# Performance work log

Hardware: AMD Instinct MI355X
Metric: run time of the kernel (lower is better)

## Reference

```python
import jax, jax.numpy as jnp
import numpy as np

N_NODES = 50000


def _add_self_loops(edge_index, num_nodes):
    loop = jnp.arange(num_nodes, dtype=edge_index.dtype)
    row = jnp.concatenate([edge_index[0], loop])
    col = jnp.concatenate([edge_index[1], loop])
    return row, col


def _gcn_norm(row, col, num_nodes):
    # deg computed on target index with unit edge weights (PyG gcn_norm)
    deg = jax.ops.segment_sum(jnp.ones_like(col, dtype=jnp.float32), col,
                              num_segments=num_nodes)
    dis = jnp.where(deg > 0, jax.lax.rsqrt(jnp.maximum(deg, 1.0)), 0.0)
    return dis[row] * dis[col]  # [E]


def _gcn_conv(x, W, b, row, col, norm, num_nodes):
    h = x @ W                                  # dense transform first (PyG order)
    msg = h[row] * norm[:, None]               # gather + normalize
    out = jax.ops.segment_sum(msg, col, num_segments=num_nodes)  # scatter-add
    return out + b


def setup_inputs() -> dict:
    key = jax.random.key(0)
    ks = jax.random.split(key, 10)
    E = 800000
    x = jax.random.normal(ks[0], (N_NODES, 29), dtype=jnp.float32)
    edge_index = jax.random.randint(ks[1], (2, E), 0, N_NODES, dtype=jnp.int64)

    def glorot(k, fan_in, fan_out):
        s = jnp.sqrt(2.0 / (fan_in + fan_out)).astype(jnp.float32)
        return jax.random.normal(k, (fan_in, fan_out), dtype=jnp.float32) * s

    return {
        "x": x, "edge_index": edge_index,
        "W1": glorot(ks[2], 29, 96),  "b1": jnp.zeros((96,), jnp.float32),
        "W2": glorot(ks[3], 96, 128), "b2": jnp.zeros((128,), jnp.float32),
        "W3": glorot(ks[4], 128, 64), "b3": jnp.zeros((64,), jnp.float32),
        "W4": glorot(ks[5], 64, 32),  "b4": jnp.zeros((32,), jnp.float32),
    }


def reference(x, edge_index, W1, b1, W2, b2, W3, b3, W4, b4):
    row, col = _add_self_loops(edge_index, N_NODES)
    norm = _gcn_norm(row, col, N_NODES)  # same graph -> same norm for all layers
    h = _gcn_conv(x, W1, b1, row, col, norm, N_NODES)
    h = jax.nn.relu(h)
    # dropout(p=0.4) is identity in eval mode
    h = _gcn_conv(h, W2, b2, row, col, norm, N_NODES)
    h = _gcn_conv(h, W3, b3, row, col, norm, N_NODES)
    h = _gcn_conv(h, W4, b4, row, col, norm, N_NODES)
    return h
```

## Files before the change

### kernel.cpp

```cpp
#include <hip/hip_runtime.h>


constexpr int NN  = 50000;
constexpr int CAP = 64;
constexpr int AGB = (NN * 8 + 255) / 256;
constexpr int C1B = (NN + 255) / 256;
constexpr int PREPB = (NN * 32 + 64 + 255) / 256;
constexpr int W34XB = 17;
constexpr int W234XB = 13;
constexpr int PGB = 128;
constexpr int SLICE = (800000 + PGB - 1) / PGB;

typedef unsigned short u16;

__global__ void place_x_kernel(const int* __restrict__ row, const int* __restrict__ col,
                               int* __restrict__ cnt, u16* __restrict__ ell, int E) {
    const int g  = blockIdx.x & 7;
    const int bi = blockIdx.x >> 3;
    const int e0 = bi * SLICE;
    int e1 = e0 + SLICE; if (e1 > E) e1 = E;
    for (int e = e0 + threadIdx.x; e < e1; e += 256) {
        const int c = col[e];
        if ((unsigned)c >= (unsigned)NN || ((c >> 6) & 7) != g) continue;
        const int r = row[e];
        if ((unsigned)r >= (unsigned)NN) continue;
        const int pos = atomicAdd(&cnt[c], 1);
        if (pos < CAP) ell[c * CAP + pos] = (u16)r;
    }
}

__global__ void prep_all_kernel(const int* __restrict__ cnt, u16* __restrict__ ell,
                                const float* __restrict__ x, float* __restrict__ dis,
                                float* __restrict__ Ba, float* __restrict__ Bb,
                                float* __restrict__ c1d,
                                const float* __restrict__ W3, const float* __restrict__ W4,
                                const float* __restrict__ b3,
                                float* __restrict__ W34, float* __restrict__ v1) {
    if (blockIdx.x >= PREPB) {
        const int wid = (blockIdx.x - PREPB) * 256 + threadIdx.x;
        if (wid < 4096) {
            const int r = wid >> 5, j = wid & 31;
            float a = 0.f;
#pragma unroll 8
            for (int k = 0; k < 64; ++k) a = fmaf(W3[r * 64 + k], W4[k * 32 + j], a);
            W34[wid] = a;
        } else if (wid < 4128) {
            const int j = wid - 4096;
            float a = 0.f;
#pragma unroll 8
            for (int k = 0; k < 64; ++k) a = fmaf(b3[k], W4[k * 32 + j], a);
            v1[j] = a;
        }
        return;
    }
    const int idx = blockIdx.x * blockDim.x + threadIdx.x;
    if (idx < NN * 32) {
        const int n = idx >> 5, f = idx & 31;
        int m = cnt[n]; if (m > CAP) m = CAP;
        const float d = rsqrtf((float)m + 1.0f);
        Ba[idx] = (f < 29) ? x[n * 29 + f] * d : 0.f;
        if (f == 31) dis[n] = d;
        if (f == 30) {
            int mp = (m + 7) & ~7; if (mp > CAP) mp = CAP;
            for (int k = m; k < mp; ++k) ell[n * CAP + k] = (u16)NN;
        }
    } else {
        const int i = idx - NN * 32;
        if (i < 32) { Ba[NN * 32 + i] = 0.f; Bb[NN * 32 + i] = 0.f; }
        else if (i == 32) dis[NN] = 0.f;
        else if (i == 33) c1d[NN] = 0.f;
    }
}

template<int MODE>
__device__ __forceinline__ void agg32_body(const float* __restrict__ hs,
                                           const int* __restrict__ cnt,
                                           const u16* __restrict__ ell,
                                           const float* __restrict__ dis,
                                           const float* __restrict__ c1,
                                           const float* __restrict__ c2,
                                           const float* __restrict__ v1,
                                           const float* __restrict__ v2,
                                           const float* __restrict__ bv,
                                           float* __restrict__ out) {
    const int idx = blockIdx.x * blockDim.x + threadIdx.x;
    if (idx >= NN * 8) return;
    const int n = idx >> 3, c = idx & 7;
    const float4* hpc = (const float4*)hs + c;
    float4 acc = hpc[n * 8];
    int m = cnt[n]; if (m > CAP) m = CAP;
    const int m8 = (m + 7) >> 3;
    const int4* ip = (const int4*)(ell + n * CAP);
    for (int t = 0; t < m8; ++t) {
        const int4 s = ip[t];
        const unsigned ux = (unsigned)s.x, uy = (unsigned)s.y;
        const unsigned uz = (unsigned)s.z, uw = (unsigned)s.w;
        const float4 g0 = hpc[(ux & 0xFFFFu) * 8], g1 = hpc[(ux >> 16) * 8];
        const float4 g2 = hpc[(uy & 0xFFFFu) * 8], g3 = hpc[(uy >> 16) * 8];
        const float4 g4 = hpc[(uz & 0xFFFFu) * 8], g5 = hpc[(uz >> 16) * 8];
        const float4 g6 = hpc[(uw & 0xFFFFu) * 8], g7 = hpc[(uw >> 16) * 8];
        acc.x += ((g0.x + g1.x) + (g2.x + g3.x)) + ((g4.x + g5.x) + (g6.x + g7.x));
        acc.y += ((g0.y + g1.y) + (g2.y + g3.y)) + ((g4.y + g5.y) + (g6.y + g7.y));
        acc.z += ((g0.z + g1.z) + (g2.z + g3.z)) + ((g4.z + g5.z) + (g6.z + g7.z));
        acc.w += ((g0.w + g1.w) + (g2.w + g3.w)) + ((g4.w + g5.w) + (g6.w + g7.w));
    }
    const float d = dis[n];
    float4 r;
    if (MODE == 0) {
        r.x = acc.x * d; r.y = acc.y * d; r.z = acc.z * d; r.w = acc.w * d;
    } else if (MODE == 1) {
        const float d2 = d * d;
        r.x = acc.x * d2; r.y = acc.y * d2; r.z = acc.z * d2; r.w = acc.w * d2;
    } else {
        const float a1 = c1[n], a2 = c2[n];
        const float4 w1 = ((const float4*)v1)[c];
        const float4 w2 = ((const float4*)v2)[c];
        const float4 bb = ((const float4*)bv)[c];
        r.x = fmaf(acc.x, d, fmaf(a1, w1.x, fmaf(a2, w2.x, bb.x)));
        r.y = fmaf(acc.y, d, fmaf(a1, w1.y, fmaf(a2, w2.y, bb.y)));
        r.z = fmaf(acc.z, d, fmaf(a1, w1.z, fmaf(a2, w2.z, bb.z)));
        r.w = fmaf(acc.w, d, fmaf(a1, w1.w, fmaf(a2, w2.w, bb.w)));
    }
    ((float4*)out)[idx] = r;
}

__device__ __forceinline__ void agg1_body(const float* __restrict__ in,
                                          const int* __restrict__ cnt,
                                          const u16* __restrict__ ell,
                                          const float* __restrict__ dis,
                                          float* __restrict__ out,
                                          float* __restrict__ outd, int blk0) {
    const int n = (blockIdx.x - blk0) * 256 + threadIdx.x;
    if (n >= NN) return;
    float acc = in[n];
    int m = cnt[n]; if (m > CAP) m = CAP;
    const int m8 = (m + 7) >> 3;
    const int4* ip = (const int4*)(ell + n * CAP);
    for (int t = 0; t < m8; ++t) {
        const int4 s = ip[t];
        const unsigned ux = (unsigned)s.x, uy = (unsigned)s.y;
        const unsigned uz = (unsigned)s.z, uw = (unsigned)s.w;
        acc += ((in[ux & 0xFFFFu] + in[ux >> 16]) + (in[uy & 0xFFFFu] + in[uy >> 16]))
             + ((in[uz & 0xFFFFu] + in[uz >> 16]) + (in[uw & 0xFFFFu] + in[uw >> 16]));
    }
    const float r = dis[n] * acc;
    out[n] = r;
    if (outd) outd[n] = r * dis[n];
}

__global__ void agg_pre_kernel(const float* __restrict__ Ba, const int* __restrict__ cnt,
                               const u16* __restrict__ ell, const float* __restrict__ dis,
                               float* __restrict__ Bb, float* __restrict__ c1,
                               float* __restrict__ c1d,
                               const float* __restrict__ W2, const float* __restrict__ b2,
                               const float* __restrict__ W34, float* __restrict__ W234,
                               float* __restrict__ v2) {
    if (blockIdx.x < AGB) {
        agg32_body<0>(Ba, cnt, ell, dis, nullptr, nullptr, nullptr, nullptr, nullptr, Bb);
    } else if (blockIdx.x < AGB + C1B) {
        agg1_body(dis, cnt, ell, dis, c1, c1d, AGB);
    } else {
        const int wid = (blockIdx.x - AGB - C1B) * 256 + threadIdx.x;
        if (wid < 3072) {
            const int r = wid >> 5, j = wid & 31;
            float a = 0.f;
#pragma unroll 8
            for (int k = 0; k < 128; ++k) a = fmaf(W2[r * 128 + k], W34[k * 32 + j], a);
            W234[wid] = a;
        } else if (wid < 3104) {
            const int j = wid - 3072;
            float a = 0.f;
#pragma unroll 8
            for (int k = 0; k < 128; ++k) a = fmaf(b2[k], W34[k * 32 + j], a);
            v2[j] = a;
        }
    }
}

__global__ void agg_hop1_kernel(const float* __restrict__ Ba, const int* __restrict__ cnt,
                                const u16* __restrict__ ell, const float* __restrict__ dis,
                                float* __restrict__ Bb, const float* __restrict__ c1d,
                                float* __restrict__ c2) {
    if (blockIdx.x < AGB)
        agg32_body<1>(Ba, cnt, ell, dis, nullptr, nullptr, nullptr, nullptr, nullptr, Bb);
    else
        agg1_body(c1d, cnt, ell, dis, c2, nullptr, AGB);
}

__global__ void agg_hop2_kernel(const float* __restrict__ Bb, const int* __restrict__ cnt,
                                const u16* __restrict__ ell, const float* __restrict__ dis,
                                float* __restrict__ Ba) {
    agg32_body<1>(Bb, cnt, ell, dis, nullptr, nullptr, nullptr, nullptr, nullptr, Ba);
}

__global__ void agg_hop3_kernel(const float* __restrict__ Ba, const int* __restrict__ cnt,
                                const u16* __restrict__ ell, const float* __restrict__ dis,
                                const float* __restrict__ c1, const float* __restrict__ c2,
                                const float* __restrict__ v1, const float* __restrict__ v2,
                                const float* __restrict__ bv, float* __restrict__ out) {
    agg32_body<2>(Ba, cnt, ell, dis, c1, c2, v1, v2, bv, out);
}

__global__ void __launch_bounds__(192, 2)
gemm_fused_kernel(const float* __restrict__ X, const float* __restrict__ W1,
                  const float* __restrict__ b1, const float* __restrict__ dis,
                  const float* __restrict__ W234, float* __restrict__ G) {
    constexpr int NPB = 16, RSX = 36, RSH = 104;
    __shared__ float xs[NPB * RSX];
    __shared__ float hsm[NPB * RSH];
    const int tid = threadIdx.x;
    const int n0  = blockIdx.x * NPB;

    const float4* Xv = (const float4*)(X + (size_t)n0 * 32);
    for (int i = tid; i < NPB * 8; i += 192) {
        const int nl = i >> 3, r = i & 7;
        float4 v = make_float4(0.f, 0.f, 0.f, 0.f);
        if (n0 + nl < NN) v = Xv[nl * 8 + r];
        *(float4*)(xs + nl * RSX + r * 4) = v;
    }
    __syncthreads();

    {
        const int cg = tid % 24, g = tid / 24;
        const float* x0 = xs + (2 * g) * RSX;
        const float* x1 = x0 + RSX;
        const float4* Wv = (const float4*)W1;
        float4 a0 = make_float4(0.f, 0.f, 0.f, 0.f);
        float4 a1 = make_float4(0.f, 0.f, 0.f, 0.f);
#pragma unroll
        for (int k = 0; k < 29; ++k) {
            const float4 w = Wv[k * 24 + cg];
            const float v0 = x0[k], v1 = x1[k];
            a0.x = fmaf(v0, w.x, a0.x); a0.y = fmaf(v0, w.y, a0.y);
            a0.z = fmaf(v0, w.z, a0.z); a0.w = fmaf(v0, w.w, a0.w);
            a1.x = fmaf(v1, w.x, a1.x); a1.y = fmaf(v1, w.y, a1.y);
            a1.z = fmaf(v1, w.z, a1.z); a1.w = fmaf(v1, w.w, a1.w);
        }
        const float4 bb = ((const float4*)b1)[cg];
#pragma unroll
        for (int h = 0; h < 2; ++h) {
            const int nl = 2 * g + h, node = n0 + nl;
            const float d = (node < NN) ? dis[node] : 0.f;
            const float4 a = h ? a1 : a0;
            float4 r;
            r.x = fmaxf(a.x + bb.x, 0.f) * d; r.y = fmaxf(a.y + bb.y, 0.f) * d;
            r.z = fmaxf(a.z + bb.z, 0.f) * d; r.w = fmaxf(a.w + bb.w, 0.f) * d;
            *(float4*)(hsm + nl * RSH + cg * 4) = r;
        }
    }
    __syncthreads();

    if (tid < 128) {
        const int nl = tid >> 3, cg = tid & 7;
        const float* hr = hsm + nl * RSH;
        const float4* Wv = (const float4*)W234;
        float4 a = make_float4(0.f, 0.f, 0.f, 0.f);
#pragma unroll 8
        for (int k = 0; k < 96; ++k) {
            const float4 w = Wv[k * 8 + cg];
            const float v = hr[k];
            a.x = fmaf(v, w.x, a.x); a.y = fmaf(v, w.y, a.y);
            a.z = fmaf(v, w.z, a.z); a.w = fmaf(v, w.w, a.w);
        }
        const int node = n0 + nl;
        if (node < NN) ((float4*)(G + (size_t)node * 32))[cg] = a;
    }
}

extern "C" void kernel_launch(void* const* d_in, const int* in_sizes, int n_in,
                              void* d_out, int out_size, void* d_ws, size_t ws_size,
                              hipStream_t stream) {
    const float* x  = (const float*)d_in[0];
    const int*   ei = (const int*)d_in[1];
    const float* W1 = (const float*)d_in[2]; const float* b1 = (const float*)d_in[3];
    const float* W2 = (const float*)d_in[4]; const float* b2 = (const float*)d_in[5];
    const float* W3 = (const float*)d_in[6]; const float* b3 = (const float*)d_in[7];
    const float* W4 = (const float*)d_in[8]; const float* b4p = (const float*)d_in[9];
    float* outp = (float*)d_out;

    const int E = in_sizes[1] / 2;
    const int* row = ei;
    const int* col = ei + E;

    int*   cnt  = (int*)d_ws;
    float* dis  = (float*)(cnt + 50048);
    u16*   ell  = (u16*)(dis + 50056);
    float* c1   = (float*)((int*)ell + 1600000);
    float* c1d  = c1 + 50056;
    float* c2   = c1d + 50056;
    float* W34  = c2 + 50056;
    float* W234 = W34 + 4096;
    float* v1   = W234 + 3072;
    float* v2   = v1 + 32;
    float* Ba   = v2 + 32;
    float* Bb   = Ba + 1600064;

    hipMemsetAsync(cnt, 0, 50048 * sizeof(int), stream);
    place_x_kernel<<<8 * PGB, 256, 0, stream>>>(row, col, cnt, ell, E);
    prep_all_kernel<<<PREPB + W34XB, 256, 0, stream>>>(cnt, ell, x, dis, Ba, Bb, c1d,
                                                       W3, W4, b3, W34, v1);
    agg_pre_kernel<<<AGB + C1B + W234XB, 256, 0, stream>>>(Ba, cnt, ell, dis, Bb, c1, c1d,
                                                           W2, b2, W34, W234, v2);
    gemm_fused_kernel<<<(NN + 15) / 16, 192, 0, stream>>>(Bb, W1, b1, dis, W234, Ba);
    agg_hop1_kernel<<<AGB + C1B, 256, 0, stream>>>(Ba, cnt, ell, dis, Bb, c1d, c2);
    agg_hop2_kernel<<<AGB, 256, 0, stream>>>(Bb, cnt, ell, dis, Ba);
    agg_hop3_kernel<<<AGB, 256, 0, stream>>>(Ba, cnt, ell, dis, c1, c2, v1, v2, b4p, outp);
}
```

Before: 222.3 us.

## Fuse first aggregation with dense GEMMs and shift weight precompute earlier

Merges the first-layer neighbor aggregation and the fused W1/W234 dense transform into one kernel, using shared memory per 32-node block. This removes one launch and the global round trip of the aggregated features. To make W234 ready before that kernel, the W3·W4 product moves into the edge-placement kernel and the W2·W34 product moves into the prep kernel. Ping-pong buffer roles are swapped to match. The cost is a heavier per-block body with two barriers, which may lower occupancy.

```diff
diff --git a/kernel.cpp b/kernel.cpp
--- a/kernel.cpp
+++ b/kernel.cpp
@@ -4,6 +4,7 @@
 constexpr int NN  = 50000;
 constexpr int CAP = 64;
 constexpr int AGB = (NN * 8 + 255) / 256;
+constexpr int AGB32 = (NN + 31) / 32;
 constexpr int C1B = (NN + 255) / 256;
 constexpr int PREPB = (NN * 32 + 64 + 255) / 256;
 constexpr int W34XB = 17;
@@ -14,7 +15,27 @@
 typedef unsigned short u16;
 
 __global__ void place_x_kernel(const int* __restrict__ row, const int* __restrict__ col,
-                               int* __restrict__ cnt, u16* __restrict__ ell, int E) {
+                               int* __restrict__ cnt, u16* __restrict__ ell, int E,
+                               const float* __restrict__ W3, const float* __restrict__ W4,
+                               const float* __restrict__ b3,
+                               float* __restrict__ W34, float* __restrict__ v1) {
+    if (blockIdx.x >= 8 * PGB) {
+        const int wid = (blockIdx.x - 8 * PGB) * 256 + threadIdx.x;
+        if (wid < 4096) {
+            const int r = wid >> 5, j = wid & 31;
+            float a = 0.f;
+#pragma unroll 8
+            for (int k = 0; k < 64; ++k) a = fmaf(W3[r * 64 + k], W4[k * 32 + j], a);
+            W34[wid] = a;
+        } else if (wid < 4128) {
+            const int j = wid - 4096;
+            float a = 0.f;
+#pragma unroll 8
+            for (int k = 0; k < 64; ++k) a = fmaf(b3[k], W4[k * 32 + j], a);
+            v1[j] = a;
+        }
+        return;
+    }
     const int g  = blockIdx.x & 7;
     const int bi = blockIdx.x >> 3;
     const int e0 = bi * SLICE;
@@ -33,23 +54,23 @@
                                 const float* __restrict__ x, float* __restrict__ dis,
                                 float* __restrict__ Ba, float* __restrict__ Bb,
                                 float* __restrict__ c1d,
-                                const float* __restrict__ W3, const float* __restrict__ W4,
-                                const float* __restrict__ b3,
-                                float* __restrict__ W34, float* __restrict__ v1) {
+                                const float* __restrict__ W2, const float* __restrict__ b2,
+                                const float* __restrict__ W34,
+                                float* __restrict__ W234, float* __restrict__ v2) {
     if (blockIdx.x >= PREPB) {
         const int wid = (blockIdx.x - PREPB) * 256 + threadIdx.x;
-        if (wid < 4096) {
+        if (wid < 3072) {
             const int r = wid >> 5, j = wid & 31;
             float a = 0.f;
 #pragma unroll 8
-            for (int k = 0; k < 64; ++k) a = fmaf(W3[r * 64 + k], W4[k * 32 + j], a);
-            W34[wid] = a;
-        } else if (wid < 4128) {
-            const int j = wid - 4096;
+            for (int k = 0; k < 128; ++k) a = fmaf(W2[r * 128 + k], W34[k * 32 + j], a);
+            W234[wid] = a;
+        } else if (wid < 3104) {
+            const int j = wid - 3072;
             float a = 0.f;
 #pragma unroll 8
-            for (int k = 0; k < 64; ++k) a = fmaf(b3[k], W4[k * 32 + j], a);
-            v1[j] = a;
+            for (int k = 0; k < 128; ++k) a = fmaf(b2[k], W34[k * 32 + j], a);
+            v2[j] = a;
         }
         return;
     }
@@ -90,7 +111,7 @@
     float4 acc = hpc[n * 8];
     int m = cnt[n]; if (m > CAP) m = CAP;
     const int m8 = (m + 7) >> 3;
-    const int4* ip = (const int4*)(ell + n * CAP);
+    const int4* ip = (const int4*)(ell + (size_t)n * CAP);
     for (int t = 0; t < m8; ++t) {
         const int4 s = ip[t];
         const unsigned ux = (unsigned)s.x, uy = (unsigned)s.y;
@@ -135,7 +156,7 @@
     float acc = in[n];
     int m = cnt[n]; if (m > CAP) m = CAP;
     const int m8 = (m + 7) >> 3;
-    const int4* ip = (const int4*)(ell + n * CAP);
+    const int4* ip = (const int4*)(ell + (size_t)n * CAP);
     for (int t = 0; t < m8; ++t) {
         const int4 s = ip[t];
         const unsigned ux = (unsigned)s.x, uy = (unsigned)s.y;
@@ -148,32 +169,93 @@
     if (outd) outd[n] = r * dis[n];
 }
 
-__global__ void agg_pre_kernel(const float* __restrict__ Ba, const int* __restrict__ cnt,
-                               const u16* __restrict__ ell, const float* __restrict__ dis,
-                               float* __restrict__ Bb, float* __restrict__ c1,
-                               float* __restrict__ c1d,
-                               const float* __restrict__ W2, const float* __restrict__ b2,
-                               const float* __restrict__ W34, float* __restrict__ W234,
-                               float* __restrict__ v2) {
-    if (blockIdx.x < AGB) {
-        agg32_body<0>(Ba, cnt, ell, dis, nullptr, nullptr, nullptr, nullptr, nullptr, Bb);
-    } else if (blockIdx.x < AGB + C1B) {
-        agg1_body(dis, cnt, ell, dis, c1, c1d, AGB);
-    } else {
-        const int wid = (blockIdx.x - AGB - C1B) * 256 + threadIdx.x;
-        if (wid < 3072) {
-            const int r = wid >> 5, j = wid & 31;
-            float a = 0.f;
-#pragma unroll 8
-            for (int k = 0; k < 128; ++k) a = fmaf(W2[r * 128 + k], W34[k * 32 + j], a);
-            W234[wid] = a;
-        } else if (wid < 3104) {
-            const int j = wid - 3072;
-            float a = 0.f;
-#pragma unroll 8
-            for (int k = 0; k < 128; ++k) a = fmaf(b2[k], W34[k * 32 + j], a);
-            v2[j] = a;
-        }
+__global__ void __launch_bounds__(256, 4)
+agg_gemm_kernel(const float* __restrict__ Ba, const int* __restrict__ cnt,
+                const u16* __restrict__ ell, const float* __restrict__ dis,
+                const float* __restrict__ W1, const float* __restrict__ b1,
+                const float* __restrict__ W234, float* __restrict__ G,
+                float* __restrict__ c1, float* __restrict__ c1d) {
+    if (blockIdx.x >= AGB32) {
+        agg1_body(dis, cnt, ell, dis, c1, c1d, AGB32);
+        return;
+    }
+    constexpr int RSX = 40, RSH = 104;
+    __shared__ float xs[32 * RSX];
+    __shared__ float hsm[32 * RSH];
+    const int t = threadIdx.x;
+    const int nl = t >> 3, c = t & 7;
+    const int n = blockIdx.x * 32 + nl;
+
+    float4 r = make_float4(0.f, 0.f, 0.f, 0.f);
+    if (n < NN) {
+        const float4* hpc = (const float4*)Ba + c;
+        float4 acc = hpc[n * 8];
+        int m = cnt[n]; if (m > CAP) m = CAP;
+        const int m8 = (m + 7) >> 3;
+        const int4* ip = (const int4*)(ell + (size_t)n * CAP);
+        for (int tt = 0; tt < m8; ++tt) {
+            const int4 s = ip[tt];
+            const unsigned ux = (unsigned)s.x, uy = (unsigned)s.y;
+            const unsigned uz = (unsigned)s.z, uw = (unsigned)s.w;
+            const float4 g0 = hpc[(ux & 0xFFFFu) * 8], g1 = hpc[(ux >> 16) * 8];
+            const float4 g2 = hpc[(uy & 0xFFFFu) * 8], g3 = hpc[(uy >> 16) * 8];
+            const float4 g4 = hpc[(uz & 0xFFFFu) * 8], g5 = hpc[(uz >> 16) * 8];
+            const float4 g6 = hpc[(uw & 0xFFFFu) * 8], g7 = hpc[(uw >> 16) * 8];
+            acc.x += ((g0.x + g1.x) + (g2.x + g3.x)) + ((g4.x + g5.x) + (g6.x + g7.x));
+            acc.y += ((g0.y + g1.y) + (g2.y + g3.y)) + ((g4.y + g5.y) + (g6.y + g7.y));
+            acc.z += ((g0.z + g1.z) + (g2.z + g3.z)) + ((g4.z + g5.z) + (g6.z + g7.z));
+            acc.w += ((g0.w + g1.w) + (g2.w + g3.w)) + ((g4.w + g5.w) + (g6.w + g7.w));
+        }
+        const float d = dis[n];
+        r.x = acc.x * d; r.y = acc.y * d; r.z = acc.z * d; r.w = acc.w * d;
+    }
+    *(float4*)(xs + nl * RSX + c * 4) = r;
+    __syncthreads();
+
+    {
+        const float* xr = xs + nl * RSX;
+        const float4* Wv = (const float4*)W1;
+        float4 a0 = make_float4(0.f, 0.f, 0.f, 0.f);
+        float4 a1 = make_float4(0.f, 0.f, 0.f, 0.f);
+        float4 a2 = make_float4(0.f, 0.f, 0.f, 0.f);
+#pragma unroll
+        for (int k = 0; k < 29; ++k) {
+            const float xv = xr[k];
+            const float4 w0 = Wv[k * 24 + c * 3 + 0];
+            const float4 w1w = Wv[k * 24 + c * 3 + 1];
+            const float4 w2w = Wv[k * 24 + c * 3 + 2];
+            a0.x = fmaf(xv, w0.x, a0.x); a0.y = fmaf(xv, w0.y, a0.y);
+            a0.z = fmaf(xv, w0.z, a0.z); a0.w = fmaf(xv, w0.w, a0.w);
+            a1.x = fmaf(xv, w1w.x, a1.x); a1.y = fmaf(xv, w1w.y, a1.y);
+            a1.z = fmaf(xv, w1w.z, a1.z); a1.w = fmaf(xv, w1w.w, a1.w);
+            a2.x = fmaf(xv, w2w.x, a2.x); a2.y = fmaf(xv, w2w.y, a2.y);
+            a2.z = fmaf(xv, w2w.z, a2.z); a2.w = fmaf(xv, w2w.w, a2.w);
+        }
+        const float d = (n < NN) ? dis[n] : 0.f;
+#pragma unroll
+        for (int j = 0; j < 3; ++j) {
+            const float4 a = (j == 0) ? a0 : (j == 1) ? a1 : a2;
+            const float4 bb = ((const float4*)b1)[c * 3 + j];
+            float4 h;
+            h.x = fmaxf(a.x + bb.x, 0.f) * d; h.y = fmaxf(a.y + bb.y, 0.f) * d;
+            h.z = fmaxf(a.z + bb.z, 0.f) * d; h.w = fmaxf(a.w + bb.w, 0.f) * d;
+            *(float4*)(hsm + nl * RSH + (c * 3 + j) * 4) = h;
+        }
+    }
+    __syncthreads();
+
+    {
+        const float* hr = hsm + nl * RSH;
+        const float4* Wv = (const float4*)W234;
+        float4 a = make_float4(0.f, 0.f, 0.f, 0.f);
+#pragma unroll 8
+        for (int k = 0; k < 96; ++k) {
+            const float4 w = Wv[k * 8 + c];
+            const float v = hr[k];
+            a.x = fmaf(v, w.x, a.x); a.y = fmaf(v, w.y, a.y);
+            a.z = fmaf(v, w.z, a.z); a.w = fmaf(v, w.w, a.w);
+        }
+        if (n < NN) ((float4*)(G + (size_t)n * 32))[c] = a;
     }
 }
 
@@ -199,72 +281,6 @@
                                 const float* __restrict__ v1, const float* __restrict__ v2,
                                 const float* __restrict__ bv, float* __restrict__ out) {
     agg32_body<2>(Ba, cnt, ell, dis, c1, c2, v1, v2, bv, out);
-}
-
-__global__ void __launch_bounds__(192, 2)
-gemm_fused_kernel(const float* __restrict__ X, const float* __restrict__ W1,
-                  const float* __restrict__ b1, const float* __restrict__ dis,
-                  const float* __restrict__ W234, float* __restrict__ G) {
-    constexpr int NPB = 16, RSX = 36, RSH = 104;
-    __shared__ float xs[NPB * RSX];
-    __shared__ float hsm[NPB * RSH];
-    const int tid = threadIdx.x;
-    const int n0  = blockIdx.x * NPB;
-
-    const float4* Xv = (const float4*)(X + (size_t)n0 * 32);
-    for (int i = tid; i < NPB * 8; i += 192) {
-        const int nl = i >> 3, r = i & 7;
-        float4 v = make_float4(0.f, 0.f, 0.f, 0.f);
-        if (n0 + nl < NN) v = Xv[nl * 8 + r];
-        *(float4*)(xs + nl * RSX + r * 4) = v;
-    }
-    __syncthreads();
-
-    {
-        const int cg = tid % 24, g = tid / 24;
-        const float* x0 = xs + (2 * g) * RSX;
-        const float* x1 = x0 + RSX;
-        const float4* Wv = (const float4*)W1;
-        float4 a0 = make_float4(0.f, 0.f, 0.f, 0.f);
-        float4 a1 = make_float4(0.f, 0.f, 0.f, 0.f);
-#pragma unroll
-        for (int k = 0; k < 29; ++k) {
-            const float4 w = Wv[k * 24 + cg];
-            const float v0 = x0[k], v1 = x1[k];
-            a0.x = fmaf(v0, w.x, a0.x); a0.y = fmaf(v0, w.y, a0.y);
-            a0.z = fmaf(v0, w.z, a0.z); a0.w = fmaf(v0, w.w, a0.w);
-            a1.x = fmaf(v1, w.x, a1.x); a1.y = fmaf(v1, w.y, a1.y);
-            a1.z = fmaf(v1, w.z, a1.z); a1.w = fmaf(v1, w.w, a1.w);
-        }
-        const float4 bb = ((const float4*)b1)[cg];
-#pragma unroll
-        for (int h = 0; h < 2; ++h) {
-            const int nl = 2 * g + h, node = n0 + nl;
-            const float d = (node < NN) ? dis[node] : 0.f;
-            const float4 a = h ? a1 : a0;
-            float4 r;
-            r.x = fmaxf(a.x + bb.x, 0.f) * d; r.y = fmaxf(a.y + bb.y, 0.f) * d;
-            r.z = fmaxf(a.z + bb.z, 0.f) * d; r.w = fmaxf(a.w + bb.w, 0.f) * d;
-            *(float4*)(hsm + nl * RSH + cg * 4) = r;
-        }
-    }
-    __syncthreads();
-
-    if (tid < 128) {
-        const int nl = tid >> 3, cg = tid & 7;
-        const float* hr = hsm + nl * RSH;
-        const float4* Wv = (const float4*)W234;
-        float4 a = make_float4(0.f, 0.f, 0.f, 0.f);
-#pragma unroll 8
-        for (int k = 0; k < 96; ++k) {
-            const float4 w = Wv[k * 8 + cg];
-            const float v = hr[k];
-            a.x = fmaf(v, w.x, a.x); a.y = fmaf(v, w.y, a.y);
-            a.z = fmaf(v, w.z, a.z); a.w = fmaf(v, w.w, a.w);
-        }
-        const int node = n0 + nl;
-        if (node < NN) ((float4*)(G + (size_t)node * 32))[cg] = a;
-    }
 }
 
 extern "C" void kernel_launch(void* const* d_in, const int* in_sizes, int n_in,
@@ -296,13 +312,13 @@
     float* Bb   = Ba + 1600064;
 
     hipMemsetAsync(cnt, 0, 50048 * sizeof(int), stream);
-    place_x_kernel<<<8 * PGB, 256, 0, stream>>>(row, col, cnt, ell, E);
-    prep_all_kernel<<<PREPB + W34XB, 256, 0, stream>>>(cnt, ell, x, dis, Ba, Bb, c1d,
-                                                       W3, W4, b3, W34, v1);
-    agg_pre_kernel<<<AGB + C1B + W234XB, 256, 0, stream>>>(Ba, cnt, ell, dis, Bb, c1, c1d,
-                                                           W2, b2, W34, W234, v2);
-    gemm_fused_kernel<<<(NN + 15) / 16, 192, 0, stream>>>(Bb, W1, b1, dis, W234, Ba);
-    agg_hop1_kernel<<<AGB + C1B, 256, 0, stream>>>(Ba, cnt, ell, dis, Bb, c1d, c2);
-    agg_hop2_kernel<<<AGB, 256, 0, stream>>>(Bb, cnt, ell, dis, Ba);
-    agg_hop3_kernel<<<AGB, 256, 0, stream>>>(Ba, cnt, ell, dis, c1, c2, v1, v2, b4p, outp);
-}
+    place_x_kernel<<<8 * PGB + W34XB, 256, 0, stream>>>(row, col, cnt, ell, E,
+                                                        W3, W4, b3, W34, v1);
+    prep_all_kernel<<<PREPB + W234XB, 256, 0, stream>>>(cnt, ell, x, dis, Ba, Bb, c1d,
+                                                        W2, b2, W34, W234, v2);
+    agg_gemm_kernel<<<AGB32 + C1B, 256, 0, stream>>>(Ba, cnt, ell, dis,
+                                                     W1, b1, W234, Bb, c1, c1d);
+    agg_hop1_kernel<<<AGB + C1B, 256, 0, stream>>>(Bb, cnt, ell, dis, Ba, c1d, c2);
+    agg_hop2_kernel<<<AGB, 256, 0, stream>>>(Ba, cnt, ell, dis, Bb);
+    agg_hop3_kernel<<<AGB, 256, 0, stream>>>(Bb, cnt, ell, dis, c1, c2, v1, v2, b4p, outp);
+}
```

After: 431.2 us. +94.0%, slower.
